# Kernel optimization log

Hardware: AMD Instinct MI355X
Metric: run time of the kernel (lower is better)

Reference implementation:

```python
import jax, jax.numpy as jnp
import numpy as np

NEG_SLOPE = 0.1

def lrelu(x):
    return jnp.where(x >= 0, x, NEG_SLOPE * x)

def conv2d(x, w, b, padding=0, dilation=1):
    y = jax.lax.conv_general_dilated(
        x, w, window_strides=(1, 1),
        padding=[(padding, padding), (padding, padding)],
        rhs_dilation=(dilation, dilation),
        dimension_numbers=('NCHW', 'OIHW', 'NCHW'))
    return y + b[None, :, None, None]

def res_aspp(x, p):
    r1 = lrelu(conv2d(x, p['a1_w'], p['a1_b'], padding=1, dilation=1))
    r2 = lrelu(conv2d(x, p['a2_w'], p['a2_b'], padding=2, dilation=2))
    r3 = lrelu(conv2d(x, p['a3_w'], p['a3_b'], padding=4, dilation=4))
    r = conv2d(jnp.concatenate((r1, r2, r3), axis=1), p['ar_w'], p['ar_b'])
    return x + r

def deform_conv2d(x, offset, w, b):
    # x: [B,C,H,W], offset: [B,2*K,H,W] torchvision layout (y,x) per 3x3 tap
    B, C, H, W = x.shape
    KH = KW = 3
    K = KH * KW
    pad = 1
    off = offset.reshape(B, K, 2, H, W)
    ky, kx = jnp.meshgrid(jnp.arange(KH), jnp.arange(KW), indexing='ij')
    ky = ky.reshape(K).astype(x.dtype)
    kx = kx.reshape(K).astype(x.dtype)
    hh = jnp.arange(H, dtype=x.dtype)
    ww = jnp.arange(W, dtype=x.dtype)
    # sampling positions [B,K,H,W]
    py = off[:, :, 0] + (hh[None, None, :, None] - pad + ky[None, :, None, None])
    px = off[:, :, 1] + (ww[None, None, None, :] - pad + kx[None, :, None, None])
    y0 = jnp.floor(py)
    x0 = jnp.floor(px)
    wy = (py - y0)[:, None]  # [B,1,K,H,W]
    wx = (px - x0)[:, None]
    y0i = y0.astype(jnp.int32)
    x0i = x0.astype(jnp.int32)
    x_flat = x.reshape(B, C, H * W)

    def gather(iy, ix):
        valid = ((iy >= 0) & (iy < H) & (ix >= 0) & (ix < W)).astype(x.dtype)
        idx = jnp.clip(iy, 0, H - 1) * W + jnp.clip(ix, 0, W - 1)  # [B,K,H,W]
        v = jax.vmap(lambda xb, ib: xb[:, ib])(x_flat, idx.reshape(B, -1))
        return v.reshape(B, C, K, H, W) * valid[:, None]

    samp = (gather(y0i, x0i) * (1 - wy) * (1 - wx)
            + gather(y0i, x0i + 1) * (1 - wy) * wx
            + gather(y0i + 1, x0i) * wy * (1 - wx)
            + gather(y0i + 1, x0i + 1) * wy * wx)
    out = jnp.einsum('bckhw,ock->bohw', samp, w.reshape(w.shape[0], C, K))
    return out + b[None, :, None, None]

def setup_inputs() -> dict:
    key = jax.random.key(0)
    ks = jax.random.split(key, 16)
    B, C, H, W = 4, 64, 160, 160
    Cout = 64
    s = 0.05
    d = {
        'in_aux': jax.random.normal(ks[0], (B, C, H, W), jnp.float32),
        'in_ref': jax.random.normal(ks[1], (B, C, H, W), jnp.float32),
        'w01': jax.random.normal(ks[2], (Cout, 2 * C, 1, 1), jnp.float32) * s,
        'b01': jnp.zeros((Cout,), jnp.float32),
        'a1_w': jax.random.normal(ks[3], (Cout, Cout, 3, 3), jnp.float32) * s,
        'a1_b': jnp.zeros((Cout,), jnp.float32),
        'a2_w': jax.random.normal(ks[4], (Cout, Cout, 3, 3), jnp.float32) * s,
        'a2_b': jnp.zeros((Cout,), jnp.float32),
        'a3_w': jax.random.normal(ks[5], (Cout, Cout, 3, 3), jnp.float32) * s,
        'a3_b': jnp.zeros((Cout,), jnp.float32),
        'ar_w': jax.random.normal(ks[6], (Cout, 3 * Cout, 1, 1), jnp.float32) * s,
        'ar_b': jnp.zeros((Cout,), jnp.float32),
        'w02': jax.random.normal(ks[7], (18, Cout, 1, 1), jnp.float32) * s,
        'b02': jnp.zeros((18,), jnp.float32),
        'dw': jax.random.normal(ks[8], (Cout, C, 3, 3), jnp.float32) * s,
        'db': jnp.zeros((Cout,), jnp.float32),
    }
    return d

def reference(in_aux, in_ref, w01, b01, a1_w, a1_b, a2_w, a2_b, a3_w, a3_b,
              ar_w, ar_b, w02, b02, dw, db):
    cat_x = jnp.concatenate((in_aux, in_ref), axis=1)
    off_x = lrelu(conv2d(cat_x, w01, b01))
    p = {'a1_w': a1_w, 'a1_b': a1_b, 'a2_w': a2_w, 'a2_b': a2_b,
         'a3_w': a3_w, 'a3_b': a3_b, 'ar_w': ar_w, 'ar_b': ar_b}
    off_x = res_aspp(off_x, p)
    off_x = conv2d(off_x, w02, b02)
    return deform_conv2d(in_aux, off_x, dw, db)
```

## Files before the change

kernel.cpp:

```cpp
#include <hip/hip_runtime.h>
#include <math.h>

static constexpr int B = 4, H = 160, W = 160;
static constexpr int HW = H * W;
static constexpr int CHW = 64 * HW;
static constexpr int NELEM = B * CHW;

typedef short bf16x8 __attribute__((ext_vector_type(8)));
typedef float f32x4 __attribute__((ext_vector_type(4)));

__device__ __forceinline__ float lrelu(float v) { return v >= 0.f ? v : 0.1f * v; }

__device__ __forceinline__ unsigned short f2bf(float f) {
  unsigned u = __float_as_uint(f);
  return (unsigned short)((u + 0x7FFFu + ((u >> 16) & 1u)) >> 16);
}
__device__ __forceinline__ float bf2f(short u) {
  return __uint_as_float(((unsigned)(unsigned short)u) << 16);
}

__global__ __launch_bounds__(256) void k_transform(
    const float* __restrict__ w01, const float* __restrict__ dw,
    const float* __restrict__ arw, const float* __restrict__ a1w,
    const float* __restrict__ a2w, const float* __restrict__ a3w,
    float* __restrict__ wt01, float* __restrict__ arwT,
    unsigned short* __restrict__ wb_bf, unsigned short* __restrict__ wd_bf) {
  int i = blockIdx.x * 256 + threadIdx.x;
  if (i < 8192) {
    int ci = i >> 6, o = i & 63;
    wt01[i] = w01[o * 128 + ci];
  } else if (i < 20480) {
    int j = i - 8192;
    int cp = j >> 6, o = j & 63;
    arwT[j] = arw[o * 192 + cp];
  } else if (i < 131072) {
    int j = i - 20480;
    int ci = j & 63, co = (j >> 6) & 63;
    int kk = j >> 12;
    int dsel = kk / 9; kk -= dsel * 9;
    const float* src = dsel == 0 ? a1w : dsel == 1 ? a2w : a3w;
    wb_bf[j] = f2bf(src[(co * 64 + ci) * 9 + kk]);
  } else if (i < 167936) {
    int j = i - 131072;
    int ci = j & 63, co = (j >> 6) & 63, k = j >> 12;
    wd_bf[j] = f2bf(dw[(co * 64 + ci) * 9 + k]);
  }
}

__global__ __launch_bounds__(256) void k_conv1x1_in(
    const float* __restrict__ aux, const float* __restrict__ ref,
    const float* __restrict__ wt01, const float* __restrict__ b01,
    float* __restrict__ out, unsigned short* __restrict__ out_bf) {
  __shared__ float s[128 * 64];
  int pos0 = blockIdx.x * 64;
  int b = pos0 / HW;
  int hw0 = pos0 - b * HW;
  int tid = threadIdx.x;
  for (int i = tid; i < 8192; i += 256) {
    int ci = i >> 6, p = i & 63;
    const float* src = (ci < 64) ? (aux + b * CHW + ci * HW)
                                 : (ref + b * CHW + (ci - 64) * HW);
    s[i] = src[hw0 + p];
  }
  __syncthreads();
  int p = tid & 63;
  int g = __builtin_amdgcn_readfirstlane(tid >> 6);
  const float* wp = wt01 + g * 16;
  float acc[16];
#pragma unroll
  for (int j = 0; j < 16; ++j) acc[j] = 0.f;
#pragma unroll 4
  for (int ci = 0; ci < 128; ++ci) {
    float sv = s[ci * 64 + p];
    const float* wrow = wp + ci * 64;
#pragma unroll
    for (int j = 0; j < 16; ++j) acc[j] += sv * wrow[j];
  }
  const float* bb = b01 + g * 16;
  int obase = (b * 64 + g * 16) * HW + hw0 + p;
  unsigned short tb[16];
#pragma unroll
  for (int j = 0; j < 16; ++j) {
    float v = lrelu(acc[j] + bb[j]);
    out[obase + j * HW] = v;
    tb[j] = f2bf(v);
  }
  unsigned short* dst = out_bf + ((size_t)(b * HW + hw0 + p)) * 64 + g * 16;
  *(uint4*)dst = *(const uint4*)&tb[0];
  *(uint4*)(dst + 8) = *(const uint4*)&tb[8];
}

__global__ __launch_bounds__(256) void k_aspp3_mfma(
    const unsigned short* __restrict__ off0_bf,
    const unsigned short* __restrict__ wb_bf,
    const float* __restrict__ a1b, const float* __restrict__ a2b,
    const float* __restrict__ a3b,
    float* __restrict__ r1, float* __restrict__ r2, float* __restrict__ r3) {
  __shared__ unsigned short sin[576 * 40];
  int bx = blockIdx.x, by = blockIdx.y;
  int dsel = blockIdx.z >> 2, b = blockIdx.z & 3;
  int d = 1 << dsel;
  const float* bias = dsel == 0 ? a1b : dsel == 1 ? a2b : a3b;
  float* rout = dsel == 0 ? r1 : dsel == 1 ? r2 : r3;
  int tid = threadIdx.x;
  int lane = tid & 63, wid = tid >> 6;
  int m = lane & 15, q = lane >> 4;
  f32x4 acc[4][4] = {};
  const unsigned short* wbase = wb_bf + dsel * 9 * 4096;

  for (int ch = 0; ch < 2; ++ch) {
    __syncthreads();
    for (int i = tid; i < 2304; i += 256) {
      int pix = i >> 2, sub = i & 3;
      int py = pix / 24, px = pix - py * 24;
      int gy = by * 16 + py - 4, gx = bx * 16 + px - 4;
      uint4 v = make_uint4(0u, 0u, 0u, 0u);
      if (gy >= 0 && gy < H && gx >= 0 && gx < W)
        v = *(const uint4*)(off0_bf +
                            ((size_t)(b * HW + gy * W + gx)) * 64 + ch * 32 + sub * 8);
      *(uint4*)(sin + pix * 40 + sub * 8) = v;
    }
    __syncthreads();
#pragma unroll
    for (int k = 0; k < 9; ++k) {
      int ky = k / 3, kx = k - ky * 3;
      bf16x8 bfrag[4];
#pragma unroll
      for (int t = 0; t < 4; ++t)
        bfrag[t] = *(const bf16x8*)(wbase + ((k * 64 + t * 16 + m) * 64) + ch * 32 + q * 8);
      bf16x8 afrag[4];
#pragma unroll
      for (int mt = 0; mt < 4; ++mt) {
        int row = 4 + wid * 4 + mt + (ky - 1) * d;
        int col = 4 + m + (kx - 1) * d;
        afrag[mt] = *(const bf16x8*)(sin + (row * 24 + col) * 40 + q * 8);
      }
#pragma unroll
      for (int mt = 0; mt < 4; ++mt)
#pragma unroll
        for (int t = 0; t < 4; ++t)
          acc[mt][t] = __builtin_amdgcn_mfma_f32_16x16x32_bf16(
              afrag[mt], bfrag[t], acc[mt][t], 0, 0, 0);
    }
  }

  float* ep = (float*)sin;
  for (int hp = 0; hp < 2; ++hp) {
    __syncthreads();
#pragma unroll
    for (int t2 = 0; t2 < 2; ++t2) {
      int t = hp * 2 + t2;
#pragma unroll
      for (int mt = 0; mt < 4; ++mt) {
        int prow = wid * 4 + mt;
#pragma unroll
        for (int r = 0; r < 4; ++r) {
          int pix = prow * 16 + q * 4 + r;
          ep[pix * 33 + t2 * 16 + m] = acc[mt][t][r];
        }
      }
    }
    __syncthreads();
    for (int it = 0; it < 32; ++it) {
      int c = it, pix = tid;
      int prow = pix >> 4, pcol = pix & 15;
      int co = hp * 32 + c;
      float v = ep[pix * 33 + c] + bias[co];
      rout[((size_t)(b * 64 + co)) * HW + (by * 16 + prow) * W + bx * 16 + pcol] =
          lrelu(v);
    }
  }
}

__global__ __launch_bounds__(256) void k_merge_head(
    const float* __restrict__ r1, const float* __restrict__ r2,
    const float* __restrict__ r3, const float* __restrict__ off0,
    const float* __restrict__ arwT, const float* __restrict__ arb,
    const float* __restrict__ w02, const float* __restrict__ b02,
    float* __restrict__ offs) {
  __shared__ float s[192 * 64];
  int pos0 = blockIdx.x * 64;
  int b = pos0 / HW;
  int hw0 = pos0 - b * HW;
  int tid = threadIdx.x;
  for (int i = tid; i < 4096; i += 256) {
    int c = i >> 6, p = i & 63;
    int gidx = (b * 64 + c) * HW + hw0 + p;
    s[i] = r1[gidx];
    s[4096 + i] = r2[gidx];
    s[8192 + i] = r3[gidx];
  }
  __syncthreads();
  int p = tid & 63;
  int g = __builtin_amdgcn_readfirstlane(tid >> 6);
  float macc[16];
#pragma unroll
  for (int j = 0; j < 16; ++j)
    macc[j] = arb[g * 16 + j] + off0[(b * 64 + g * 16 + j) * HW + hw0 + p];
#pragma unroll 4
  for (int cp = 0; cp < 192; ++cp) {
    float sv = s[cp * 64 + p];
    const float* arow = arwT + cp * 64 + g * 16;
#pragma unroll
    for (int j = 0; j < 16; ++j) macc[j] += sv * arow[j];
  }
  __syncthreads();
#pragma unroll
  for (int j = 0; j < 16; ++j) s[(g * 16 + j) * 64 + p] = macc[j];
  __syncthreads();
  for (int i = tid; i < 1152; i += 256) {
    int t = i >> 6, pp = i & 63;
    const float* w2 = w02 + t * 64;
    float o = b02[t];
#pragma unroll 8
    for (int co = 0; co < 64; ++co) o += s[co * 64 + pp] * w2[co];
    offs[(b * 18 + t) * HW + hw0 + pp] = o;
  }
}

__global__ __launch_bounds__(256) void k_xbf(
    const float* __restrict__ aux, unsigned short* __restrict__ x_bf) {
  __shared__ float s[64 * 64];
  int pos0 = blockIdx.x * 64;
  int b = pos0 / HW;
  int hw0 = pos0 - b * HW;
  int tid = threadIdx.x;
  for (int i = tid; i < 4096; i += 256) {
    int ci = i >> 6, p = i & 63;
    s[i] = aux[b * CHW + ci * HW + hw0 + p];
  }
  __syncthreads();
  int p = tid & 63, g = tid >> 6;
  unsigned short tb[16];
#pragma unroll
  for (int j = 0; j < 16; ++j) tb[j] = f2bf(s[(g * 16 + j) * 64 + p]);
  unsigned short* dst = x_bf + ((size_t)(b * HW + hw0 + p)) * 64 + g * 16;
  *(uint4*)dst = *(const uint4*)&tb[0];
  *(uint4*)(dst + 8) = *(const uint4*)&tb[8];
}

__global__ __launch_bounds__(256) void k_deform_mfma(
    const unsigned short* __restrict__ x_bf, const float* __restrict__ offs,
    const unsigned short* __restrict__ wd_bf, const float* __restrict__ db,
    float* __restrict__ out) {
  constexpr int SP = 72;
  __shared__ unsigned short sb[2][64 * SP];
  int blk = (blockIdx.x & 7) * 200 + (blockIdx.x >> 3);
  int pos0 = blk * 64;
  int b = pos0 / HW;
  int hw0 = pos0 - b * HW;
  int tid = threadIdx.x;
  int lane = tid & 63, wid = tid >> 6;
  int m = lane & 15, q = lane >> 4;
  int p = lane;
  int cg = wid;
  int hw = hw0 + p;
  int h = hw / W, wv = hw - h * W;
  const unsigned short* xb = x_bf + (size_t)b * HW * 64;
  const float* ob = offs + b * 18 * HW + hw;
  float offv[18];
#pragma unroll
  for (int j = 0; j < 18; ++j) offv[j] = ob[j * HW];
  f32x4 acc[4] = {};

#pragma unroll
  for (int k = 0; k < 9; ++k) {
    const int ky = k / 3, kx = k - ky * 3;
    float py = offv[2 * k] + (float)(h - 1 + ky);
    float px = offv[2 * k + 1] + (float)(wv - 1 + kx);
    float fy = floorf(py), fx = floorf(px);
    int iy0 = (int)fy, ix0 = (int)fx;
    float wy = py - fy, wx = px - fx;
    int iy1 = iy0 + 1, ix1 = ix0 + 1;
    float vy0 = (iy0 >= 0 && iy0 < H) ? 1.f : 0.f;
    float vy1 = (iy1 >= 0 && iy1 < H) ? 1.f : 0.f;
    float vx0 = (ix0 >= 0 && ix0 < W) ? 1.f : 0.f;
    float vx1 = (ix1 >= 0 && ix1 < W) ? 1.f : 0.f;
    int cy0 = min(max(iy0, 0), H - 1), cy1 = min(max(iy1, 0), H - 1);
    int cx0 = min(max(ix0, 0), W - 1), cx1 = min(max(ix1, 0), W - 1);
    float c00 = vy0 * vx0 * (1.f - wy) * (1.f - wx);
    float c01 = vy0 * vx1 * (1.f - wy) * wx;
    float c10 = vy1 * vx0 * wy * (1.f - wx);
    float c11 = vy1 * vx1 * wy * wx;
    const unsigned short* p00 = xb + (size_t)(cy0 * W + cx0) * 64 + cg * 16;
    const unsigned short* p01 = xb + (size_t)(cy0 * W + cx1) * 64 + cg * 16;
    const unsigned short* p10 = xb + (size_t)(cy1 * W + cx0) * 64 + cg * 16;
    const unsigned short* p11 = xb + (size_t)(cy1 * W + cx1) * 64 + cg * 16;
    unsigned short tb[16];
#pragma unroll
    for (int c2 = 0; c2 < 2; ++c2) {
      bf16x8 v00 = *(const bf16x8*)(p00 + c2 * 8);
      bf16x8 v01 = *(const bf16x8*)(p01 + c2 * 8);
      bf16x8 v10 = *(const bf16x8*)(p10 + c2 * 8);
      bf16x8 v11 = *(const bf16x8*)(p11 + c2 * 8);
#pragma unroll
      for (int j = 0; j < 8; ++j) {
        float sv = c00 * bf2f(v00[j]) + c01 * bf2f(v01[j]) +
                   c10 * bf2f(v10[j]) + c11 * bf2f(v11[j]);
        tb[c2 * 8 + j] = f2bf(sv);
      }
    }
    unsigned short* wr = &sb[k & 1][p * SP + cg * 16];
    *(uint4*)wr = *(const uint4*)&tb[0];
    *(uint4*)(wr + 8) = *(const uint4*)&tb[8];
    __syncthreads();
    const unsigned short* rb = &sb[k & 1][0];
#pragma unroll
    for (int kc = 0; kc < 2; ++kc) {
      bf16x8 bfrag =
          *(const bf16x8*)(wd_bf + (k * 64 + wid * 16 + m) * 64 + kc * 32 + q * 8);
#pragma unroll
      for (int mt = 0; mt < 4; ++mt) {
        bf16x8 afrag = *(const bf16x8*)(rb + (mt * 16 + m) * SP + kc * 32 + q * 8);
        acc[mt] = __builtin_amdgcn_mfma_f32_16x16x32_bf16(afrag, bfrag, acc[mt],
                                                          0, 0, 0);
      }
    }
  }
  int co = wid * 16 + m;
  float bias = db[co];
  size_t orow = (size_t)(b * 64 + co) * HW + hw0;
#pragma unroll
  for (int mt = 0; mt < 4; ++mt)
#pragma unroll
    for (int r = 0; r < 4; ++r)
      out[orow + mt * 16 + q * 4 + r] = acc[mt][r] + bias;
}

extern "C" void kernel_launch(void* const* d_in, const int* in_sizes, int n_in,
                              void* d_out, int out_size, void* d_ws, size_t ws_size,
                              hipStream_t stream) {
  const float* aux = (const float*)d_in[0];
  const float* ref = (const float*)d_in[1];
  const float* w01 = (const float*)d_in[2];
  const float* b01 = (const float*)d_in[3];
  const float* a1w = (const float*)d_in[4];
  const float* a1b = (const float*)d_in[5];
  const float* a2w = (const float*)d_in[6];
  const float* a2b = (const float*)d_in[7];
  const float* a3w = (const float*)d_in[8];
  const float* a3b = (const float*)d_in[9];
  const float* arw = (const float*)d_in[10];
  const float* arb = (const float*)d_in[11];
  const float* w02 = (const float*)d_in[12];
  const float* b02 = (const float*)d_in[13];
  const float* dw  = (const float*)d_in[14];
  const float* db  = (const float*)d_in[15];
  float* out = (float*)d_out;

  float* off0 = (float*)d_ws;
  float* r1   = off0 + NELEM;
  float* r2   = r1 + NELEM;
  float* r3   = r2 + NELEM;
  float* offs = r3 + NELEM;
  float* wt01 = offs + B * 18 * HW;
  float* arwT = wt01 + 8192;
  unsigned short* off0_bf = (unsigned short*)(arwT + 12288);
  unsigned short* wb_bf = off0_bf + (size_t)NELEM;
  unsigned short* wd_bf = wb_bf + 110592;
  unsigned short* x_bf = (unsigned short*)r1;

  k_transform<<<656, 256, 0, stream>>>(w01, dw, arw, a1w, a2w, a3w,
                                       wt01, arwT, wb_bf, wd_bf);
  k_conv1x1_in<<<B * HW / 64, 256, 0, stream>>>(aux, ref, wt01, b01, off0,
                                                off0_bf);
  k_aspp3_mfma<<<dim3(10, 10, 12), 256, 0, stream>>>(
      off0_bf, wb_bf, a1b, a2b, a3b, r1, r2, r3);
  k_merge_head<<<B * HW / 64, 256, 0, stream>>>(
      r1, r2, r3, off0, arwT, arb, w02, b02, offs);
  k_xbf<<<B * HW / 64, 256, 0, stream>>>(aux, x_bf);
  k_deform_mfma<<<B * HW / 64, 256, 0, stream>>>(x_bf, offs, wd_bf, db, out);
}
```

Measured before the change: 378.6 us.

## Store ASPP branches as channel-last bf16 and run merge conv on MFMA

The ASPP kernel now applies bias and leaky ReLU in its epilogue and writes r1/r2/r3 as one interleaved bf16 NHWC buffer (192 channels per pixel) in place of three fp32 NCHW tensors. The 192-to-64 merge conv becomes an MFMA bf16 GEMM that reads this buffer and adds the fp32 residual. The bf16 conversion of aux is folded into the first 1x1 conv kernel, so the separate k_xbf launch is gone. This cuts intermediate memory traffic and one launch, at the cost of bf16 rounding in the merge inputs and weights.

```diff
diff --git a/kernel.cpp b/kernel.cpp
--- a/kernel.cpp
+++ b/kernel.cpp
@@ -23,34 +23,34 @@
     const float* __restrict__ w01, const float* __restrict__ dw,
     const float* __restrict__ arw, const float* __restrict__ a1w,
     const float* __restrict__ a2w, const float* __restrict__ a3w,
-    float* __restrict__ wt01, float* __restrict__ arwT,
-    unsigned short* __restrict__ wb_bf, unsigned short* __restrict__ wd_bf) {
+    float* __restrict__ wt01, unsigned short* __restrict__ wb_bf,
+    unsigned short* __restrict__ wd_bf, unsigned short* __restrict__ arw_bf) {
   int i = blockIdx.x * 256 + threadIdx.x;
   if (i < 8192) {
     int ci = i >> 6, o = i & 63;
     wt01[i] = w01[o * 128 + ci];
-  } else if (i < 20480) {
+  } else if (i < 118784) {
     int j = i - 8192;
-    int cp = j >> 6, o = j & 63;
-    arwT[j] = arw[o * 192 + cp];
-  } else if (i < 131072) {
-    int j = i - 20480;
     int ci = j & 63, co = (j >> 6) & 63;
     int kk = j >> 12;
     int dsel = kk / 9; kk -= dsel * 9;
     const float* src = dsel == 0 ? a1w : dsel == 1 ? a2w : a3w;
     wb_bf[j] = f2bf(src[(co * 64 + ci) * 9 + kk]);
-  } else if (i < 167936) {
-    int j = i - 131072;
+  } else if (i < 155648) {
+    int j = i - 118784;
     int ci = j & 63, co = (j >> 6) & 63, k = j >> 12;
     wd_bf[j] = f2bf(dw[(co * 64 + ci) * 9 + k]);
+  } else if (i < 167936) {
+    int j = i - 155648;
+    arw_bf[j] = f2bf(arw[j]);
   }
 }
 
 __global__ __launch_bounds__(256) void k_conv1x1_in(
     const float* __restrict__ aux, const float* __restrict__ ref,
     const float* __restrict__ wt01, const float* __restrict__ b01,
-    float* __restrict__ out, unsigned short* __restrict__ out_bf) {
+    float* __restrict__ out, unsigned short* __restrict__ out_bf,
+    unsigned short* __restrict__ x_bf) {
   __shared__ float s[128 * 64];
   int pos0 = blockIdx.x * 64;
   int b = pos0 / HW;
@@ -88,20 +88,24 @@
   unsigned short* dst = out_bf + ((size_t)(b * HW + hw0 + p)) * 64 + g * 16;
   *(uint4*)dst = *(const uint4*)&tb[0];
   *(uint4*)(dst + 8) = *(const uint4*)&tb[8];
+  unsigned short xb[16];
+#pragma unroll
+  for (int j = 0; j < 16; ++j) xb[j] = f2bf(s[(g * 16 + j) * 64 + p]);
+  unsigned short* xdst = x_bf + ((size_t)(b * HW + hw0 + p)) * 64 + g * 16;
+  *(uint4*)xdst = *(const uint4*)&xb[0];
+  *(uint4*)(xdst + 8) = *(const uint4*)&xb[8];
 }
 
 __global__ __launch_bounds__(256) void k_aspp3_mfma(
     const unsigned short* __restrict__ off0_bf,
     const unsigned short* __restrict__ wb_bf,
     const float* __restrict__ a1b, const float* __restrict__ a2b,
-    const float* __restrict__ a3b,
-    float* __restrict__ r1, float* __restrict__ r2, float* __restrict__ r3) {
+    const float* __restrict__ a3b, unsigned short* __restrict__ r_bf) {
   __shared__ unsigned short sin[576 * 40];
   int bx = blockIdx.x, by = blockIdx.y;
   int dsel = blockIdx.z >> 2, b = blockIdx.z & 3;
   int d = 1 << dsel;
   const float* bias = dsel == 0 ? a1b : dsel == 1 ? a2b : a3b;
-  float* rout = dsel == 0 ? r1 : dsel == 1 ? r2 : r3;
   int tid = threadIdx.x;
   int lane = tid & 63, wid = tid >> 6;
   int m = lane & 15, q = lane >> 4;
@@ -144,99 +148,85 @@
     }
   }
 
-  float* ep = (float*)sin;
-  for (int hp = 0; hp < 2; ++hp) {
-    __syncthreads();
-#pragma unroll
-    for (int t2 = 0; t2 < 2; ++t2) {
-      int t = hp * 2 + t2;
-#pragma unroll
-      for (int mt = 0; mt < 4; ++mt) {
-        int prow = wid * 4 + mt;
-#pragma unroll
-        for (int r = 0; r < 4; ++r) {
-          int pix = prow * 16 + q * 4 + r;
-          ep[pix * 33 + t2 * 16 + m] = acc[mt][t][r];
-        }
+  unsigned short* epb = sin;
+  __syncthreads();
+#pragma unroll
+  for (int t = 0; t < 4; ++t) {
+    float bi = bias[t * 16 + m];
+#pragma unroll
+    for (int mt = 0; mt < 4; ++mt) {
+      int prow = wid * 4 + mt;
+#pragma unroll
+      for (int r = 0; r < 4; ++r) {
+        int pix = prow * 16 + q * 4 + r;
+        epb[pix * 72 + t * 16 + m] = f2bf(lrelu(acc[mt][t][r] + bi));
       }
     }
-    __syncthreads();
-    for (int it = 0; it < 32; ++it) {
-      int c = it, pix = tid;
-      int prow = pix >> 4, pcol = pix & 15;
-      int co = hp * 32 + c;
-      float v = ep[pix * 33 + c] + bias[co];
-      rout[((size_t)(b * 64 + co)) * HW + (by * 16 + prow) * W + bx * 16 + pcol] =
-          lrelu(v);
-    }
-  }
-}
-
-__global__ __launch_bounds__(256) void k_merge_head(
-    const float* __restrict__ r1, const float* __restrict__ r2,
-    const float* __restrict__ r3, const float* __restrict__ off0,
-    const float* __restrict__ arwT, const float* __restrict__ arb,
+  }
+  __syncthreads();
+  {
+    int pix = tid;
+    int prow = pix >> 4, pcol = pix & 15;
+    unsigned short* dst =
+        r_bf + ((size_t)(b * HW + (by * 16 + prow) * W + bx * 16 + pcol)) * 192 +
+        dsel * 64;
+    const unsigned short* src = epb + pix * 72;
+#pragma unroll
+    for (int c = 0; c < 8; ++c)
+      *(uint4*)(dst + c * 8) = *(const uint4*)(src + c * 8);
+  }
+}
+
+__global__ __launch_bounds__(256) void k_merge_head_mfma(
+    const unsigned short* __restrict__ r_bf, const float* __restrict__ off0,
+    const unsigned short* __restrict__ arw_bf, const float* __restrict__ arb,
     const float* __restrict__ w02, const float* __restrict__ b02,
     float* __restrict__ offs) {
-  __shared__ float s[192 * 64];
+  __shared__ unsigned short sa[64 * 200];
   int pos0 = blockIdx.x * 64;
   int b = pos0 / HW;
   int hw0 = pos0 - b * HW;
   int tid = threadIdx.x;
-  for (int i = tid; i < 4096; i += 256) {
-    int c = i >> 6, p = i & 63;
-    int gidx = (b * 64 + c) * HW + hw0 + p;
-    s[i] = r1[gidx];
-    s[4096 + i] = r2[gidx];
-    s[8192 + i] = r3[gidx];
-  }
-  __syncthreads();
-  int p = tid & 63;
-  int g = __builtin_amdgcn_readfirstlane(tid >> 6);
-  float macc[16];
-#pragma unroll
-  for (int j = 0; j < 16; ++j)
-    macc[j] = arb[g * 16 + j] + off0[(b * 64 + g * 16 + j) * HW + hw0 + p];
-#pragma unroll 4
-  for (int cp = 0; cp < 192; ++cp) {
-    float sv = s[cp * 64 + p];
-    const float* arow = arwT + cp * 64 + g * 16;
-#pragma unroll
-    for (int j = 0; j < 16; ++j) macc[j] += sv * arow[j];
-  }
-  __syncthreads();
-#pragma unroll
-  for (int j = 0; j < 16; ++j) s[(g * 16 + j) * 64 + p] = macc[j];
+  const unsigned short* gsrc = r_bf + (size_t)(b * HW + hw0) * 192;
+  for (int i = tid; i < 1536; i += 256) {
+    int pos = i / 24, c8 = i - pos * 24;
+    *(uint4*)(sa + pos * 200 + c8 * 8) = *(const uint4*)(gsrc + i * 8);
+  }
+  __syncthreads();
+  int lane = tid & 63, wid = tid >> 6;
+  int m = lane & 15, q = lane >> 4;
+  f32x4 acc[4] = {};
+#pragma unroll
+  for (int kc = 0; kc < 6; ++kc) {
+    bf16x8 bfrag = *(const bf16x8*)(arw_bf + (wid * 16 + m) * 192 + kc * 32 + q * 8);
+#pragma unroll
+    for (int mt = 0; mt < 4; ++mt) {
+      bf16x8 afrag = *(const bf16x8*)(sa + (mt * 16 + m) * 200 + kc * 32 + q * 8);
+      acc[mt] = __builtin_amdgcn_mfma_f32_16x16x32_bf16(afrag, bfrag, acc[mt],
+                                                        0, 0, 0);
+    }
+  }
+  __syncthreads();
+  float* ep = (float*)sa;
+  int co = wid * 16 + m;
+  float bi = arb[co];
+  const float* resrow = off0 + (size_t)(b * 64 + co) * HW + hw0;
+#pragma unroll
+  for (int mt = 0; mt < 4; ++mt)
+#pragma unroll
+    for (int r = 0; r < 4; ++r) {
+      int pos = mt * 16 + q * 4 + r;
+      ep[pos * 65 + co] = acc[mt][r] + bi + resrow[pos];
+    }
   __syncthreads();
   for (int i = tid; i < 1152; i += 256) {
-    int t = i >> 6, pp = i & 63;
+    int t = i >> 6, p = i & 63;
     const float* w2 = w02 + t * 64;
     float o = b02[t];
 #pragma unroll 8
-    for (int co = 0; co < 64; ++co) o += s[co * 64 + pp] * w2[co];
-    offs[(b * 18 + t) * HW + hw0 + pp] = o;
-  }
-}
-
-__global__ __launch_bounds__(256) void k_xbf(
-    const float* __restrict__ aux, unsigned short* __restrict__ x_bf) {
-  __shared__ float s[64 * 64];
-  int pos0 = blockIdx.x * 64;
-  int b = pos0 / HW;
-  int hw0 = pos0 - b * HW;
-  int tid = threadIdx.x;
-  for (int i = tid; i < 4096; i += 256) {
-    int ci = i >> 6, p = i & 63;
-    s[i] = aux[b * CHW + ci * HW + hw0 + p];
-  }
-  __syncthreads();
-  int p = tid & 63, g = tid >> 6;
-  unsigned short tb[16];
-#pragma unroll
-  for (int j = 0; j < 16; ++j) tb[j] = f2bf(s[(g * 16 + j) * 64 + p]);
-  unsigned short* dst = x_bf + ((size_t)(b * HW + hw0 + p)) * 64 + g * 16;
-  *(uint4*)dst = *(const uint4*)&tb[0];
-  *(uint4*)(dst + 8) = *(const uint4*)&tb[8];
+    for (int c = 0; c < 64; ++c) o += ep[p * 65 + c] * w2[c];
+    offs[(b * 18 + t) * HW + hw0 + p] = o;
+  }
 }
 
 __global__ __launch_bounds__(256) void k_deform_mfma(
@@ -349,25 +339,22 @@
   float* out = (float*)d_out;
 
   float* off0 = (float*)d_ws;
-  float* r1   = off0 + NELEM;
-  float* r2   = r1 + NELEM;
-  float* r3   = r2 + NELEM;
-  float* offs = r3 + NELEM;
+  float* offs = off0 + NELEM;
   float* wt01 = offs + B * 18 * HW;
-  float* arwT = wt01 + 8192;
-  unsigned short* off0_bf = (unsigned short*)(arwT + 12288);
-  unsigned short* wb_bf = off0_bf + (size_t)NELEM;
-  unsigned short* wd_bf = wb_bf + 110592;
-  unsigned short* x_bf = (unsigned short*)r1;
+  unsigned short* off0_bf = (unsigned short*)(wt01 + 8192);
+  unsigned short* x_bf   = off0_bf + (size_t)NELEM;
+  unsigned short* wb_bf  = x_bf + (size_t)NELEM;
+  unsigned short* wd_bf  = wb_bf + 110592;
+  unsigned short* arw_bf = wd_bf + 36864;
+  unsigned short* r_bf   = arw_bf + 12288;
 
   k_transform<<<656, 256, 0, stream>>>(w01, dw, arw, a1w, a2w, a3w,
-                                       wt01, arwT, wb_bf, wd_bf);
+                                       wt01, wb_bf, wd_bf, arw_bf);
   k_conv1x1_in<<<B * HW / 64, 256, 0, stream>>>(aux, ref, wt01, b01, off0,
-                                                off0_bf);
+                                                off0_bf, x_bf);
   k_aspp3_mfma<<<dim3(10, 10, 12), 256, 0, stream>>>(
-      off0_bf, wb_bf, a1b, a2b, a3b, r1, r2, r3);
-  k_merge_head<<<B * HW / 64, 256, 0, stream>>>(
-      r1, r2, r3, off0, arwT, arb, w02, b02, offs);
-  k_xbf<<<B * HW / 64, 256, 0, stream>>>(aux, x_bf);
+      off0_bf, wb_bf, a1b, a2b, a3b, r_bf);
+  k_merge_head_mfma<<<B * HW / 64, 256, 0, stream>>>(
+      r_bf, off0, arw_bf, arb, w02, b02, offs);
   k_deform_mfma<<<B * HW / 64, 256, 0, stream>>>(x_bf, offs, wd_bf, db, out);
 }
```

Measured after the change: 333.3 us. -12.0%, faster.
